# Optimization experiments

Measured on AMD Instinct MI355X. Metric: run time of the kernel, lower is better.

Reference implementation:

```python
import jax, jax.numpy as jnp
import numpy as np

ROPE_BASE = 10000.0

def rope_2d(x, h, w):
    # x: (b, h, w, c); 2D RoPE, first half of pair-channels rotated by row angle, second by col angle
    b, _, _, c = x.shape
    k_max = c // 4  # c // (2 * num_spatial_dims)
    theta = 1.0 / (ROPE_BASE ** (jnp.arange(k_max, dtype=jnp.float32) / k_max))  # (k_max,)
    ang_h = jnp.arange(h, dtype=jnp.float32)[:, None] * theta  # (h, k_max)
    ang_w = jnp.arange(w, dtype=jnp.float32)[:, None] * theta  # (w, k_max)
    # angles: (h, w, 2*k_max) = cat([i*theta, j*theta], -1)
    angles = jnp.concatenate([
        jnp.broadcast_to(ang_h[:, None, :], (h, w, k_max)),
        jnp.broadcast_to(ang_w[None, :, :], (h, w, k_max)),
    ], axis=-1)
    cos = jnp.cos(angles)  # (h, w, c//2)
    sin = jnp.sin(angles)
    xr = x[..., 0::2]  # consecutive-pair real parts (b,h,w,c//2)
    xi = x[..., 1::2]
    out_r = xr * cos - xi * sin
    out_i = xr * sin + xi * cos
    return jnp.stack([out_r, out_i], axis=-1).reshape(b, h, w, c)

def linear_attention_fwd(x, h, w, qk_w, qk_b, lepe_w, lepe_b, num_heads=4):
    b, n, c = x.shape
    head_dim = c // num_heads
    qk = x @ qk_w.T + qk_b  # (b, n, 2c)
    q, k = qk[..., :c], qk[..., c:]
    v = x
    q = jax.nn.elu(q) + 1.0
    k = jax.nn.elu(k) + 1.0
    q_rope = rope_2d(q.reshape(b, h, w, c), h, w).reshape(b, n, num_heads, head_dim).transpose(0, 2, 1, 3)
    k_rope = rope_2d(k.reshape(b, h, w, c), h, w).reshape(b, n, num_heads, head_dim).transpose(0, 2, 1, 3)
    qh = q.reshape(b, n, num_heads, head_dim).transpose(0, 2, 1, 3)  # (b,H,n,d)
    kh = k.reshape(b, n, num_heads, head_dim).transpose(0, 2, 1, 3)
    vh = v.reshape(b, n, num_heads, head_dim).transpose(0, 2, 1, 3)
    k_mean = kh.mean(axis=2)  # (b,H,d)
    z = 1.0 / (jnp.einsum('bhnd,bhd->bhn', qh, k_mean) + 1e-6)  # (b,H,n)
    inv_n = 1.0 / n
    kv = jnp.einsum('bhnd,bhne->bhde', k_rope, vh) * inv_n  # (b,H,d,d)
    out = jnp.einsum('bhnd,bhde->bhne', q_rope, kv) * z[..., None]  # (b,H,n,d)
    out = out.transpose(0, 2, 1, 3).reshape(b, n, c)
    # LePE: depthwise 3x3 conv on v in NCHW
    v_img = v.reshape(b, h, w, c).transpose(0, 3, 1, 2)  # (b,c,h,w)
    lepe = jax.lax.conv_general_dilated(
        v_img, lepe_w, window_strides=(1, 1), padding='SAME',
        feature_group_count=c, dimension_numbers=('NCHW', 'OIHW', 'NCHW'))
    lepe = lepe + lepe_b[None, :, None, None]
    out = out + lepe.transpose(0, 2, 3, 1).reshape(b, n, c)
    return out.transpose(0, 2, 1).reshape(b, c, h, w)

def setup_inputs() -> dict:
    key = jax.random.key(0)
    ks = jax.random.split(key, 5)
    b, h, w, c = 16, 128, 128, 64
    n = h * w
    x = jax.random.normal(ks[0], (b, n, c), dtype=jnp.float32)
    qk_w = jax.random.normal(ks[1], (2 * c, c), dtype=jnp.float32) * (1.0 / np.sqrt(c))
    qk_b = jax.random.normal(ks[2], (2 * c,), dtype=jnp.float32) * 0.02
    lepe_w = jax.random.normal(ks[3], (c, 1, 3, 3), dtype=jnp.float32) * (1.0 / 3.0)
    lepe_b = jax.random.normal(ks[4], (c,), dtype=jnp.float32) * 0.02
    return {"x": x, "h": h, "w": w, "qk_w": qk_w, "qk_b": qk_b, "lepe_w": lepe_w, "lepe_b": lepe_b}

def reference(x, h, w, qk_w, qk_b, lepe_w, lepe_b):
    return linear_attention_fwd(x, h, w, qk_w, qk_b, lepe_w, lepe_b, num_heads=4)
```

## Files before the change

### kernel.cpp

```cpp
#include <hip/hip_runtime.h>

#define B_   16
#define C_   64
#define HH   128
#define WW   128
#define NN   (HH*WW)
#define NH   4
#define PADB 72
#define PADO 66

typedef short short8 __attribute__((ext_vector_type(8)));
typedef float f32x4  __attribute__((ext_vector_type(4)));

#define NEG_L2_10K_OVER16 (-0.8304820237218406f)

__device__ __forceinline__ float act_elu1(float v) {
    return v > 0.f ? v + 1.f : __expf(v);
}
__device__ __forceinline__ short f2bf(float f) {
    union { float f; unsigned u; } v; v.f = f;
    unsigned r = (v.u + 0x7FFFu + ((v.u >> 16) & 1u)) >> 16;
    return (short)r;
}
__device__ __forceinline__ float bf2f(short s) {
    union { unsigned u; float f; } v; v.u = ((unsigned)(unsigned short)s) << 16;
    return v.f;
}
__device__ __forceinline__ unsigned cvt2bf(float lo, float hi) {
    unsigned r;
    asm("v_cvt_pk_bf16_f32 %0, %1, %2" : "=v"(r) : "v"(lo), "v"(hi));
    return r;
}

__global__ __launch_bounds__(256) void la_init(
    const float* __restrict__ qk_w, const float* __restrict__ lepe_w,
    float2* __restrict__ g_tab, float* __restrict__ g_wT,
    short* __restrict__ g_wbf)
{
    int i = blockIdx.x * 256 + threadIdx.x;
    g_wbf[i] = f2bf(qk_w[i]);
    if (i < 2048) {
        int coord = i >> 4, t = i & 15;
        float theta = exp2f(NEG_L2_10K_OVER16 * (float)t);
        float s, c;
        __sincosf((float)coord * theta, &s, &c);
        g_tab[i] = make_float2(c, s);
    }
    if (i < 576) {
        int tap = i >> 6, ch = i & 63;
        g_wT[i] = lepe_w[ch * 9 + tap];
    }
}

__global__ __launch_bounds__(256) void la_phase1(
    const float* __restrict__ x, const float* __restrict__ qk_b,
    const short* __restrict__ g_wbf, const float2* __restrict__ g_tab,
    float* __restrict__ g_part, short* __restrict__ g_q)
{
    __shared__ __align__(16) char pool[3*64*PADB*2 + 256*4];
    short* sXT = (short*)pool;
    short* sKT = sXT + 64*PADB;
    short* sQ  = sKT + 64*PADB;
    float* kmp = (float*)(sQ + 64*PADB);

    const int tid  = threadIdx.x;
    const int w    = tid >> 6;
    const int ln   = tid & 15;
    const int quad = (tid >> 4) & 3;
    const int b    = blockIdx.y;
    const int nblk = blockIdx.x;
    const float* xb = x + (size_t)b * (size_t)(NN * C_);

    float biasK[4], biasQ[4];
    #pragma unroll
    for (int nt = 0; nt < 4; ++nt) {
        biasK[nt] = qk_b[64 + 16*nt + ln];
        biasQ[nt] = qk_b[16*nt + ln];
    }

    f32x4 acc2 = {0.f, 0.f, 0.f, 0.f};
    float kmacc[4] = {0.f, 0.f, 0.f, 0.f};

    for (int ck = 0; ck < 4; ++ck) {
        const int n0 = nblk*256 + ck*64;
        if (ck) __syncthreads();
        #pragma unroll
        for (int it = 0; it < 4; ++it) {
            int idx = tid + 256*it;
            int row = idx & 63, k4 = (idx >> 6) << 2;
            float4 xv = *(const float4*)(xb + (size_t)(n0 + row)*C_ + k4);
            unsigned p01 = cvt2bf(xv.x, xv.y), p23 = cvt2bf(xv.z, xv.w);
            sXT[(k4+0)*PADB + row] = (short)p01;
            sXT[(k4+1)*PADB + row] = (short)(p01 >> 16);
            sXT[(k4+2)*PADB + row] = (short)p23;
            sXT[(k4+3)*PADB + row] = (short)(p23 >> 16);
        }
        short8 aF[2];
        #pragma unroll
        for (int ks = 0; ks < 2; ++ks) {
            const float* ap = xb + (size_t)(n0 + 16*w + ln)*C_ + 32*ks + 8*quad;
            float4 a0 = *(const float4*)ap;
            float4 a1 = *(const float4*)(ap + 4);
            union { unsigned u[4]; short8 s; } af;
            af.u[0] = cvt2bf(a0.x, a0.y);
            af.u[1] = cvt2bf(a0.z, a0.w);
            af.u[2] = cvt2bf(a1.x, a1.y);
            af.u[3] = cvt2bf(a1.z, a1.w);
            aF[ks] = af.s;
        }
        f32x4 ak[4], aq[4];
        #pragma unroll
        for (int nt = 0; nt < 4; ++nt) { ak[nt] = (f32x4){0.f,0.f,0.f,0.f}; aq[nt] = (f32x4){0.f,0.f,0.f,0.f}; }
        #pragma unroll
        for (int ks = 0; ks < 2; ++ks) {
            #pragma unroll
            for (int nt = 0; nt < 4; ++nt) {
                short8 bk = *(const short8*)(g_wbf + (64 + 16*nt + ln)*C_ + 32*ks + 8*quad);
                short8 bq = *(const short8*)(g_wbf + (16*nt + ln)*C_ + 32*ks + 8*quad);
                ak[nt] = __builtin_amdgcn_mfma_f32_16x16x32_bf16(aF[ks], bk, ak[nt], 0, 0, 0);
                aq[nt] = __builtin_amdgcn_mfma_f32_16x16x32_bf16(aF[ks], bq, aq[nt], 0, 0, 0);
            }
        }
        const int ycoord = n0 >> 7;
        const int x0 = n0 & 127;
        #pragma unroll
        for (int nt = 0; nt < 4; ++nt) {
            const int j = 16*nt + ln;
            const int t = j >> 1;
            const float sgn = (j & 1) ? 1.f : -1.f;
            float2 cs_y;
            if (nt < 2) cs_y = g_tab[ycoord*16 + t];
            #pragma unroll
            for (int r = 0; r < 4; ++r) {
                int p_loc = 16*w + 4*quad + r;
                float kval = act_elu1(ak[nt][r] + biasK[nt]);
                kmacc[nt] += kval;
                float P = __shfl_xor(kval, 1);
                float2 cs = (nt < 2) ? cs_y : g_tab[(x0 + p_loc)*16 + (t - 16)];
                float kr = kval*cs.x + sgn*P*cs.y;
                sKT[j*PADB + p_loc] = f2bf(kr);
                float qval = act_elu1(aq[nt][r] + biasQ[nt]);
                sQ[p_loc*PADB + j] = f2bf(qval);
            }
        }
        __syncthreads();
        #pragma unroll
        for (int ks = 0; ks < 2; ++ks) {
            short8 a  = *(const short8*)(sKT + (16*w + ln)*PADB + 32*ks + 8*quad);
            short8 bf = *(const short8*)(sXT + (16*w + ln)*PADB + 32*ks + 8*quad);
            acc2 = __builtin_amdgcn_mfma_f32_16x16x32_bf16(a, bf, acc2, 0, 0, 0);
        }
        #pragma unroll
        for (int cp = 0; cp < 2; ++cp) {
            int idx = tid + 256*cp;
            int row = idx >> 3, c8 = idx & 7;
            short8 qv = *(const short8*)(sQ + row*PADB + 8*c8);
            *(short8*)(g_q + ((size_t)b*NN + n0 + row)*C_ + 8*c8) = qv;
        }
    }

    float* pb = g_part + (size_t)(b*64 + nblk) * 1088;
    #pragma unroll
    for (int r = 0; r < 4; ++r)
        pb[w*256 + (4*quad + r)*16 + ln] = acc2[r];

    #pragma unroll
    for (int nt = 0; nt < 4; ++nt) {
        float v = kmacc[nt];
        v += __shfl_xor(v, 16);
        v += __shfl_xor(v, 32);
        if ((tid & 63) < 16) kmp[w*64 + 16*nt + ln] = v;
    }
    __syncthreads();
    if (tid < 64)
        pb[1024 + tid] = kmp[tid] + kmp[64 + tid] + kmp[128 + tid] + kmp[192 + tid];
}

__global__ __launch_bounds__(256) void la_reduce(
    const float* __restrict__ g_part, float* __restrict__ g_kv,
    float* __restrict__ g_km)
{
    int o = blockIdx.x * 256 + threadIdx.x;
    int b = o / 1088;
    int i = o - b * 1088;
    const float* p = g_part + (size_t)(b*64) * 1088 + i;
    float s = 0.f;
    #pragma unroll 8
    for (int nb = 0; nb < 64; ++nb) s += p[(size_t)nb * 1088];
    if (i < 1024) g_kv[b*1024 + i] = s;
    else          g_km[b*64 + (i - 1024)] = s;
}

__global__ __launch_bounds__(256) void la_phase2(
    const float* __restrict__ x, const short* __restrict__ g_q,
    const float* __restrict__ g_kv, const float* __restrict__ g_km,
    const float2* __restrict__ g_tab, const float* __restrict__ g_wT,
    const float* __restrict__ lepe_b, float* __restrict__ out)
{
    __shared__ __align__(16) char pool[64*40*2 + 64*PADO*4];
    short* sKVB = (short*)pool;
    float* sOut = (float*)(pool + 64*40*2);

    const int tid  = threadIdx.x;
    const int w    = tid >> 6;
    const int ln   = tid & 15;
    const int quad = (tid >> 4) & 3;
    const int b    = blockIdx.y;
    const int n0   = blockIdx.x * 64;
    const float* xb = x + (size_t)b * (size_t)(NN * C_);
    const float inv_n = 1.f / (float)NN;

    for (int idx = tid; idx < 1024; idx += 256) {
        int h = idx >> 8, d = (idx >> 4) & 15, e = idx & 15;
        float v = g_kv[b*1024 + idx] * inv_n;
        int rowb = h*16 + e;
        int kpos  = (h & 1) ? 16 + d : d;
        int kzero = (h & 1) ? d : 16 + d;
        sKVB[rowb*40 + kpos]  = f2bf(v);
        sKVB[rowb*40 + kzero] = 0;
    }

    const int pos    = n0 + 16*w + ln;
    const int ycoord = n0 >> 7;
    const int xcoord = (n0 & 127) + 16*w + ln;
    const short* qp = g_q + ((size_t)b*NN + pos)*C_;
    short8 q0 = *(const short8*)(qp + 8*quad);
    short8 q1 = *(const short8*)(qp + 32 + 8*quad);
    float qa[8], qb[8];
    #pragma unroll
    for (int i = 0; i < 8; ++i) { qa[i] = bf2f(q0[i]); qb[i] = bf2f(q1[i]); }

    const float* kmb = g_km + b*64;
    f32x4 km0 = *(const f32x4*)(kmb + 8*quad);
    f32x4 km1 = *(const f32x4*)(kmb + 8*quad + 4);
    f32x4 km2 = *(const f32x4*)(kmb + 32 + 8*quad);
    f32x4 km3 = *(const f32x4*)(kmb + 32 + 8*quad + 4);
    float d0 = 0.f, d1 = 0.f;
    #pragma unroll
    for (int i = 0; i < 4; ++i) {
        d0 += qa[i]*km0[i] + qa[4+i]*km1[i];
        d1 += qb[i]*km2[i] + qb[4+i]*km3[i];
    }
    d0 += __shfl_xor(d0, 16);
    d1 += __shfl_xor(d1, 16);
    const float z0 = 1.f / (d0*inv_n + 1e-6f);
    const float z1 = 1.f / (d1*inv_n + 1e-6f);

    const float* tyP = (const float*)g_tab + (ycoord*16 + 4*quad)*2;
    const float* txP = (const float*)g_tab + (xcoord*16 + 4*quad)*2;
    f32x4 ty0 = *(const f32x4*)tyP, ty1 = *(const f32x4*)(tyP + 4);
    f32x4 tx0 = *(const f32x4*)txP, tx1 = *(const f32x4*)(txP + 4);
    float cy[4] = {ty0[0], ty0[2], ty1[0], ty1[2]};
    float sy[4] = {ty0[1], ty0[3], ty1[1], ty1[3]};
    float cx[4] = {tx0[0], tx0[2], tx1[0], tx1[2]};
    float sx[4] = {tx0[1], tx0[3], tx1[1], tx1[3]};
    union { unsigned u[4]; short8 s; } A0, A1;
    #pragma unroll
    for (int p = 0; p < 4; ++p) {
        float e0 = qa[2*p], o0 = qa[2*p+1];
        A0.u[p] = cvt2bf((e0*cy[p] - o0*sy[p])*z0, (e0*sy[p] + o0*cy[p])*z0);
        float e1 = qb[2*p], o1 = qb[2*p+1];
        A1.u[p] = cvt2bf((e1*cx[p] - o1*sx[p])*z1, (e1*sx[p] + o1*cx[p])*z1);
    }

    __syncthreads();

    f32x4 accq[4];
    #pragma unroll
    for (int h = 0; h < 4; ++h) accq[h] = (f32x4){0.f,0.f,0.f,0.f};
    #pragma unroll
    for (int hh = 0; hh < 2; ++hh) {
        short8 bf0 = *(const short8*)(sKVB + (hh*16 + ln)*40 + 8*quad);
        accq[hh]   = __builtin_amdgcn_mfma_f32_16x16x32_bf16(A0.s, bf0, accq[hh], 0, 0, 0);
        short8 bf1 = *(const short8*)(sKVB + ((2+hh)*16 + ln)*40 + 8*quad);
        accq[2+hh] = __builtin_amdgcn_mfma_f32_16x16x32_bf16(A1.s, bf1, accq[2+hh], 0, 0, 0);
    }
    #pragma unroll
    for (int h = 0; h < 4; ++h)
        #pragma unroll
        for (int r = 0; r < 4; ++r)
            sOut[(16*h + ln)*PADO + 16*w + 4*quad + r] = accq[h][r];

    const int cg = tid & 15;
    const int pg = tid >> 4;
    const int p0 = 4*pg;
    const int yy = n0 >> 7, xbase = n0 & 127, gx0 = xbase + p0;
    f32x4 accl[4];
    #pragma unroll
    for (int j = 0; j < 4; ++j) accl[j] = (f32x4){0.f,0.f,0.f,0.f};
    #pragma unroll
    for (int dy = -1; dy <= 1; ++dy) {
        int y2 = yy + dy;
        if ((unsigned)y2 >= HH) continue;
        f32x4 wt0 = *(const f32x4*)(g_wT + ((dy+1)*3 + 0)*C_ + 4*cg);
        f32x4 wt1 = *(const f32x4*)(g_wT + ((dy+1)*3 + 1)*C_ + 4*cg);
        f32x4 wt2 = *(const f32x4*)(g_wT + ((dy+1)*3 + 2)*C_ + 4*cg);
        const float* rp = xb + (size_t)(y2*WW)*C_ + 4*cg;
        f32x4 cb[6];
        #pragma unroll
        for (int jj = 0; jj < 6; ++jj) {
            int col = gx0 - 1 + jj;
            cb[jj] = ((unsigned)col < WW) ? *(const f32x4*)(rp + (size_t)col*C_)
                                          : (f32x4){0.f,0.f,0.f,0.f};
        }
        #pragma unroll
        for (int j = 0; j < 4; ++j)
            accl[j] += cb[j]*wt0 + cb[j+1]*wt1 + cb[j+2]*wt2;
    }
    __syncthreads();
    #pragma unroll
    for (int j = 0; j < 4; ++j)
        #pragma unroll
        for (int i = 0; i < 4; ++i)
            sOut[(4*cg + i)*PADO + p0 + j] += accl[j][i];
    __syncthreads();

    const int ch = tid >> 2, sub = tid & 3, pp0 = 16*sub;
    const float lb = lepe_b[ch];
    float* outp = out + (size_t)b*(size_t)(C_*NN) + (size_t)ch*NN + n0 + pp0;
    #pragma unroll
    for (int g = 0; g < 4; ++g) {
        float2 a0 = *(const float2*)(sOut + ch*PADO + pp0 + 4*g);
        float2 a1 = *(const float2*)(sOut + ch*PADO + pp0 + 4*g + 2);
        float4 o4 = { a0.x + lb, a0.y + lb, a1.x + lb, a1.y + lb };
        *(float4*)(outp + 4*g) = o4;
    }
}

extern "C" void kernel_launch(void* const* d_in, const int* in_sizes, int n_in,
                              void* d_out, int out_size, void* d_ws, size_t ws_size,
                              hipStream_t stream) {
    const float* x      = (const float*)d_in[0];
    const float* qk_w   = (const float*)d_in[3];
    const float* qk_b   = (const float*)d_in[4];
    const float* lepe_w = (const float*)d_in[5];
    const float* lepe_b = (const float*)d_in[6];
    float* out = (float*)d_out;

    float*  g_part = (float*)d_ws;
    float*  g_kv   = g_part + 1024*1088;
    float*  g_km   = g_kv + 16*1024;
    float2* g_tab  = (float2*)(g_km + 16*64);
    float*  g_wT   = (float*)(g_tab + 2048);
    short*  g_wbf  = (short*)(g_wT + 576);
    short*  g_q    = (short*)(g_wbf + 8192);

    hipLaunchKernelGGL(la_init,   dim3(32),      dim3(256), 0, stream,
                       qk_w, lepe_w, g_tab, g_wT, g_wbf);
    hipLaunchKernelGGL(la_phase1, dim3(64, B_),  dim3(256), 0, stream,
                       x, qk_b, g_wbf, g_tab, g_part, g_q);
    hipLaunchKernelGGL(la_reduce, dim3(68),      dim3(256), 0, stream,
                       g_part, g_kv, g_km);
    hipLaunchKernelGGL(la_phase2, dim3(256, B_), dim3(256), 0, stream,
                       x, g_q, g_kv, g_km, g_tab, g_wT, lepe_b, out);
}
```

Before: 216.6 us.

## Recompute Q in phase2, atomically reduce KV, and drop init and reduce kernels

Phase 1 now computes only K, accumulates KV and k-mean directly with global atomics, and uses twice as many blocks. Phase 2 recomputes Q from x with its own MFMA projection, which removes the bf16 Q round trip through global memory. RoPE angles come from hardware sin/cos instead of a precomputed table, and the init and reduce kernels are replaced by a memset. The cost is redundant weight conversion in every block, extra atomic contention, and sin/cos accuracy that depends on range reduction.

```diff
diff --git a/kernel.cpp b/kernel.cpp
--- a/kernel.cpp
+++ b/kernel.cpp
@@ -5,7 +5,6 @@
 #define HH   128
 #define WW   128
 #define NN   (HH*WW)
-#define NH   4
 #define PADB 72
 #define PADO 66
 
@@ -13,6 +12,7 @@
 typedef float f32x4  __attribute__((ext_vector_type(4)));
 
 #define NEG_L2_10K_OVER16 (-0.8304820237218406f)
+#define INV2PI 0.15915494309189535f
 
 __device__ __forceinline__ float act_elu1(float v) {
     return v > 0.f ? v + 1.f : __expf(v);
@@ -22,46 +22,26 @@
     unsigned r = (v.u + 0x7FFFu + ((v.u >> 16) & 1u)) >> 16;
     return (short)r;
 }
-__device__ __forceinline__ float bf2f(short s) {
-    union { unsigned u; float f; } v; v.u = ((unsigned)(unsigned short)s) << 16;
-    return v.f;
-}
 __device__ __forceinline__ unsigned cvt2bf(float lo, float hi) {
     unsigned r;
     asm("v_cvt_pk_bf16_f32 %0, %1, %2" : "=v"(r) : "v"(lo), "v"(hi));
     return r;
 }
-
-__global__ __launch_bounds__(256) void la_init(
-    const float* __restrict__ qk_w, const float* __restrict__ lepe_w,
-    float2* __restrict__ g_tab, float* __restrict__ g_wT,
-    short* __restrict__ g_wbf)
+__device__ __forceinline__ void hw_sincos(float rev, float* s, float* c) {
+    float f = rev - floorf(rev);
+    *s = __builtin_amdgcn_sinf(f);
+    *c = __builtin_amdgcn_cosf(f);
+}
+
+__global__ __launch_bounds__(256) void la_phase1(
+    const float* __restrict__ x, const float* __restrict__ qk_w,
+    const float* __restrict__ qk_b, float* __restrict__ g_kv,
+    float* __restrict__ g_km)
 {
-    int i = blockIdx.x * 256 + threadIdx.x;
-    g_wbf[i] = f2bf(qk_w[i]);
-    if (i < 2048) {
-        int coord = i >> 4, t = i & 15;
-        float theta = exp2f(NEG_L2_10K_OVER16 * (float)t);
-        float s, c;
-        __sincosf((float)coord * theta, &s, &c);
-        g_tab[i] = make_float2(c, s);
-    }
-    if (i < 576) {
-        int tap = i >> 6, ch = i & 63;
-        g_wT[i] = lepe_w[ch * 9 + tap];
-    }
-}
-
-__global__ __launch_bounds__(256) void la_phase1(
-    const float* __restrict__ x, const float* __restrict__ qk_b,
-    const short* __restrict__ g_wbf, const float2* __restrict__ g_tab,
-    float* __restrict__ g_part, short* __restrict__ g_q)
-{
-    __shared__ __align__(16) char pool[3*64*PADB*2 + 256*4];
+    __shared__ __align__(16) char pool[2*64*PADB*2 + 256*4];
     short* sXT = (short*)pool;
     short* sKT = sXT + 64*PADB;
-    short* sQ  = sKT + 64*PADB;
-    float* kmp = (float*)(sQ + 64*PADB);
+    float* kmp = (float*)(sKT + 64*PADB);
 
     const int tid  = threadIdx.x;
     const int w    = tid >> 6;
@@ -71,18 +51,36 @@
     const int nblk = blockIdx.x;
     const float* xb = x + (size_t)b * (size_t)(NN * C_);
 
-    float biasK[4], biasQ[4];
-    #pragma unroll
-    for (int nt = 0; nt < 4; ++nt) {
-        biasK[nt] = qk_b[64 + 16*nt + ln];
-        biasQ[nt] = qk_b[16*nt + ln];
-    }
+    short8 bk[2][4];
+    #pragma unroll
+    for (int ks = 0; ks < 2; ++ks)
+        #pragma unroll
+        for (int nt = 0; nt < 4; ++nt) {
+            const float* wp = qk_w + (64 + 16*nt + ln)*C_ + 32*ks + 8*quad;
+            float4 w0 = *(const float4*)wp, w1 = *(const float4*)(wp + 4);
+            union { unsigned u[4]; short8 s; } uf;
+            uf.u[0] = cvt2bf(w0.x, w0.y); uf.u[1] = cvt2bf(w0.z, w0.w);
+            uf.u[2] = cvt2bf(w1.x, w1.y); uf.u[3] = cvt2bf(w1.z, w1.w);
+            bk[ks][nt] = uf.s;
+        }
+    float biasK[4];
+    #pragma unroll
+    for (int nt = 0; nt < 4; ++nt) biasK[nt] = qk_b[64 + 16*nt + ln];
+
+    float th[2];
+    #pragma unroll
+    for (int i = 0; i < 2; ++i)
+        th[i] = exp2f(NEG_L2_10K_OVER16 * (float)(8*i + (ln >> 1))) * INV2PI;
+    float sy[2], cy[2];
+    #pragma unroll
+    for (int i = 0; i < 2; ++i) hw_sincos((float)nblk * th[i], &sy[i], &cy[i]);
 
     f32x4 acc2 = {0.f, 0.f, 0.f, 0.f};
     float kmacc[4] = {0.f, 0.f, 0.f, 0.f};
-
-    for (int ck = 0; ck < 4; ++ck) {
-        const int n0 = nblk*256 + ck*64;
+    const int p_base = 16*w + 4*quad;
+
+    for (int ck = 0; ck < 2; ++ck) {
+        const int n0 = nblk*128 + ck*64;
         if (ck) __syncthreads();
         #pragma unroll
         for (int it = 0; it < 4; ++it) {
@@ -108,39 +106,30 @@
             af.u[3] = cvt2bf(a1.z, a1.w);
             aF[ks] = af.s;
         }
-        f32x4 ak[4], aq[4];
-        #pragma unroll
-        for (int nt = 0; nt < 4; ++nt) { ak[nt] = (f32x4){0.f,0.f,0.f,0.f}; aq[nt] = (f32x4){0.f,0.f,0.f,0.f}; }
-        #pragma unroll
-        for (int ks = 0; ks < 2; ++ks) {
+        f32x4 ak[4];
+        #pragma unroll
+        for (int nt = 0; nt < 4; ++nt) ak[nt] = (f32x4){0.f,0.f,0.f,0.f};
+        #pragma unroll
+        for (int ks = 0; ks < 2; ++ks)
             #pragma unroll
-            for (int nt = 0; nt < 4; ++nt) {
-                short8 bk = *(const short8*)(g_wbf + (64 + 16*nt + ln)*C_ + 32*ks + 8*quad);
-                short8 bq = *(const short8*)(g_wbf + (16*nt + ln)*C_ + 32*ks + 8*quad);
-                ak[nt] = __builtin_amdgcn_mfma_f32_16x16x32_bf16(aF[ks], bk, ak[nt], 0, 0, 0);
-                aq[nt] = __builtin_amdgcn_mfma_f32_16x16x32_bf16(aF[ks], bq, aq[nt], 0, 0, 0);
-            }
-        }
-        const int ycoord = n0 >> 7;
-        const int x0 = n0 & 127;
+            for (int nt = 0; nt < 4; ++nt)
+                ak[nt] = __builtin_amdgcn_mfma_f32_16x16x32_bf16(aF[ks], bk[ks][nt], ak[nt], 0, 0, 0);
+
+        const int x0 = ck*64;
         #pragma unroll
         for (int nt = 0; nt < 4; ++nt) {
             const int j = 16*nt + ln;
-            const int t = j >> 1;
             const float sgn = (j & 1) ? 1.f : -1.f;
-            float2 cs_y;
-            if (nt < 2) cs_y = g_tab[ycoord*16 + t];
             #pragma unroll
             for (int r = 0; r < 4; ++r) {
-                int p_loc = 16*w + 4*quad + r;
+                int p_loc = p_base + r;
                 float kval = act_elu1(ak[nt][r] + biasK[nt]);
                 kmacc[nt] += kval;
                 float P = __shfl_xor(kval, 1);
-                float2 cs = (nt < 2) ? cs_y : g_tab[(x0 + p_loc)*16 + (t - 16)];
-                float kr = kval*cs.x + sgn*P*cs.y;
-                sKT[j*PADB + p_loc] = f2bf(kr);
-                float qval = act_elu1(aq[nt][r] + biasQ[nt]);
-                sQ[p_loc*PADB + j] = f2bf(qval);
+                float s, c;
+                if (nt < 2) { s = sy[nt]; c = cy[nt]; }
+                else hw_sincos((float)(x0 + p_loc) * th[nt & 1], &s, &c);
+                sKT[j*PADB + p_loc] = f2bf(kval*c + sgn*P*s);
             }
         }
         __syncthreads();
@@ -150,19 +139,12 @@
             short8 bf = *(const short8*)(sXT + (16*w + ln)*PADB + 32*ks + 8*quad);
             acc2 = __builtin_amdgcn_mfma_f32_16x16x32_bf16(a, bf, acc2, 0, 0, 0);
         }
-        #pragma unroll
-        for (int cp = 0; cp < 2; ++cp) {
-            int idx = tid + 256*cp;
-            int row = idx >> 3, c8 = idx & 7;
-            short8 qv = *(const short8*)(sQ + row*PADB + 8*c8);
-            *(short8*)(g_q + ((size_t)b*NN + n0 + row)*C_ + 8*c8) = qv;
-        }
-    }
-
-    float* pb = g_part + (size_t)(b*64 + nblk) * 1088;
+    }
+
+    float* kvb = g_kv + b*1024;
     #pragma unroll
     for (int r = 0; r < 4; ++r)
-        pb[w*256 + (4*quad + r)*16 + ln] = acc2[r];
+        atomicAdd(kvb + w*256 + (4*quad + r)*16 + ln, acc2[r]);
 
     #pragma unroll
     for (int nt = 0; nt < 4; ++nt) {
@@ -173,33 +155,21 @@
     }
     __syncthreads();
     if (tid < 64)
-        pb[1024 + tid] = kmp[tid] + kmp[64 + tid] + kmp[128 + tid] + kmp[192 + tid];
-}
-
-__global__ __launch_bounds__(256) void la_reduce(
-    const float* __restrict__ g_part, float* __restrict__ g_kv,
-    float* __restrict__ g_km)
+        atomicAdd(g_km + b*64 + tid,
+                  kmp[tid] + kmp[64 + tid] + kmp[128 + tid] + kmp[192 + tid]);
+}
+
+__global__ __launch_bounds__(256) void la_phase2(
+    const float* __restrict__ x, const float* __restrict__ qk_w,
+    const float* __restrict__ qk_b, const float* __restrict__ lepe_w,
+    const float* __restrict__ lepe_b, const float* __restrict__ g_kv,
+    const float* __restrict__ g_km, float* __restrict__ out)
 {
-    int o = blockIdx.x * 256 + threadIdx.x;
-    int b = o / 1088;
-    int i = o - b * 1088;
-    const float* p = g_part + (size_t)(b*64) * 1088 + i;
-    float s = 0.f;
-    #pragma unroll 8
-    for (int nb = 0; nb < 64; ++nb) s += p[(size_t)nb * 1088];
-    if (i < 1024) g_kv[b*1024 + i] = s;
-    else          g_km[b*64 + (i - 1024)] = s;
-}
-
-__global__ __launch_bounds__(256) void la_phase2(
-    const float* __restrict__ x, const short* __restrict__ g_q,
-    const float* __restrict__ g_kv, const float* __restrict__ g_km,
-    const float2* __restrict__ g_tab, const float* __restrict__ g_wT,
-    const float* __restrict__ lepe_b, float* __restrict__ out)
-{
-    __shared__ __align__(16) char pool[64*40*2 + 64*PADO*4];
+    __shared__ __align__(16) char pool[5120 + 9216 + 16896 + 2304];
     short* sKVB = (short*)pool;
-    float* sOut = (float*)(pool + 64*40*2);
+    short* sQ   = (short*)(pool + 5120);
+    float* sOut = (float*)(pool + 5120 + 9216);
+    float* sWT  = (float*)(pool + 5120 + 9216 + 16896);
 
     const int tid  = threadIdx.x;
     const int w    = tid >> 6;
@@ -219,61 +189,114 @@
         sKVB[rowb*40 + kpos]  = f2bf(v);
         sKVB[rowb*40 + kzero] = 0;
     }
-
-    const int pos    = n0 + 16*w + ln;
+    if (tid < 144) {
+        float4 lw = *(const float4*)(lepe_w + tid*4);
+        float lwv[4] = {lw.x, lw.y, lw.z, lw.w};
+        #pragma unroll
+        for (int i = 0; i < 4; ++i) {
+            int e = tid*4 + i, ch = e / 9, tap = e - ch*9;
+            sWT[tap*64 + ch] = lwv[i];
+        }
+    }
+
+    short8 wq[2][4];
+    #pragma unroll
+    for (int ks = 0; ks < 2; ++ks)
+        #pragma unroll
+        for (int nt = 0; nt < 4; ++nt) {
+            const float* wp = qk_w + (16*nt + ln)*C_ + 32*ks + 8*quad;
+            float4 w0 = *(const float4*)wp, w1 = *(const float4*)(wp + 4);
+            union { unsigned u[4]; short8 s; } uf;
+            uf.u[0] = cvt2bf(w0.x, w0.y); uf.u[1] = cvt2bf(w0.z, w0.w);
+            uf.u[2] = cvt2bf(w1.x, w1.y); uf.u[3] = cvt2bf(w1.z, w1.w);
+            wq[ks][nt] = uf.s;
+        }
+    float biasq[4], kmv[4];
+    #pragma unroll
+    for (int nt = 0; nt < 4; ++nt) {
+        biasq[nt] = qk_b[16*nt + ln];
+        kmv[nt]   = g_km[b*64 + 16*nt + ln];
+    }
+    short8 aF[2];
+    #pragma unroll
+    for (int ks = 0; ks < 2; ++ks) {
+        const float* ap = xb + (size_t)(n0 + 16*w + ln)*C_ + 32*ks + 8*quad;
+        float4 a0 = *(const float4*)ap;
+        float4 a1 = *(const float4*)(ap + 4);
+        union { unsigned u[4]; short8 s; } af;
+        af.u[0] = cvt2bf(a0.x, a0.y);
+        af.u[1] = cvt2bf(a0.z, a0.w);
+        af.u[2] = cvt2bf(a1.x, a1.y);
+        af.u[3] = cvt2bf(a1.z, a1.w);
+        aF[ks] = af.s;
+    }
+    f32x4 aq[4];
+    #pragma unroll
+    for (int nt = 0; nt < 4; ++nt) aq[nt] = (f32x4){0.f,0.f,0.f,0.f};
+    #pragma unroll
+    for (int ks = 0; ks < 2; ++ks)
+        #pragma unroll
+        for (int nt = 0; nt < 4; ++nt)
+            aq[nt] = __builtin_amdgcn_mfma_f32_16x16x32_bf16(aF[ks], wq[ks][nt], aq[nt], 0, 0, 0);
+
+    float qv[4][4], dot[4] = {0.f, 0.f, 0.f, 0.f};
+    #pragma unroll
+    for (int nt = 0; nt < 4; ++nt)
+        #pragma unroll
+        for (int r = 0; r < 4; ++r) {
+            qv[nt][r] = act_elu1(aq[nt][r] + biasq[nt]);
+            dot[r] += qv[nt][r] * kmv[nt];
+        }
+    float zr[4];
+    #pragma unroll
+    for (int r = 0; r < 4; ++r) {
+        float d = dot[r];
+        d += __shfl_xor(d, 1);
+        d += __shfl_xor(d, 2);
+        d += __shfl_xor(d, 4);
+        d += __shfl_xor(d, 8);
+        zr[r] = 1.f / (d * inv_n + 1e-6f);
+    }
+
+    float th[2];
+    #pragma unroll
+    for (int i = 0; i < 2; ++i)
+        th[i] = exp2f(NEG_L2_10K_OVER16 * (float)(8*i + (ln >> 1))) * INV2PI;
     const int ycoord = n0 >> 7;
-    const int xcoord = (n0 & 127) + 16*w + ln;
-    const short* qp = g_q + ((size_t)b*NN + pos)*C_;
-    short8 q0 = *(const short8*)(qp + 8*quad);
-    short8 q1 = *(const short8*)(qp + 32 + 8*quad);
-    float qa[8], qb[8];
-    #pragma unroll
-    for (int i = 0; i < 8; ++i) { qa[i] = bf2f(q0[i]); qb[i] = bf2f(q1[i]); }
-
-    const float* kmb = g_km + b*64;
-    f32x4 km0 = *(const f32x4*)(kmb + 8*quad);
-    f32x4 km1 = *(const f32x4*)(kmb + 8*quad + 4);
-    f32x4 km2 = *(const f32x4*)(kmb + 32 + 8*quad);
-    f32x4 km3 = *(const f32x4*)(kmb + 32 + 8*quad + 4);
-    float d0 = 0.f, d1 = 0.f;
-    #pragma unroll
-    for (int i = 0; i < 4; ++i) {
-        d0 += qa[i]*km0[i] + qa[4+i]*km1[i];
-        d1 += qb[i]*km2[i] + qb[4+i]*km3[i];
-    }
-    d0 += __shfl_xor(d0, 16);
-    d1 += __shfl_xor(d1, 16);
-    const float z0 = 1.f / (d0*inv_n + 1e-6f);
-    const float z1 = 1.f / (d1*inv_n + 1e-6f);
-
-    const float* tyP = (const float*)g_tab + (ycoord*16 + 4*quad)*2;
-    const float* txP = (const float*)g_tab + (xcoord*16 + 4*quad)*2;
-    f32x4 ty0 = *(const f32x4*)tyP, ty1 = *(const f32x4*)(tyP + 4);
-    f32x4 tx0 = *(const f32x4*)txP, tx1 = *(const f32x4*)(txP + 4);
-    float cy[4] = {ty0[0], ty0[2], ty1[0], ty1[2]};
-    float sy[4] = {ty0[1], ty0[3], ty1[1], ty1[3]};
-    float cx[4] = {tx0[0], tx0[2], tx1[0], tx1[2]};
-    float sx[4] = {tx0[1], tx0[3], tx1[1], tx1[3]};
-    union { unsigned u[4]; short8 s; } A0, A1;
-    #pragma unroll
-    for (int p = 0; p < 4; ++p) {
-        float e0 = qa[2*p], o0 = qa[2*p+1];
-        A0.u[p] = cvt2bf((e0*cy[p] - o0*sy[p])*z0, (e0*sy[p] + o0*cy[p])*z0);
-        float e1 = qb[2*p], o1 = qb[2*p+1];
-        A1.u[p] = cvt2bf((e1*cx[p] - o1*sx[p])*z1, (e1*sx[p] + o1*cx[p])*z1);
-    }
-
+    const int x0 = n0 & 127;
+    float sy[2], cy[2];
+    #pragma unroll
+    for (int i = 0; i < 2; ++i) hw_sincos((float)ycoord * th[i], &sy[i], &cy[i]);
+    const int p_base = 16*w + 4*quad;
+    #pragma unroll
+    for (int nt = 0; nt < 4; ++nt) {
+        const int j = 16*nt + ln;
+        const float sgn = (j & 1) ? 1.f : -1.f;
+        #pragma unroll
+        for (int r = 0; r < 4; ++r) {
+            int p_loc = p_base + r;
+            float s, c;
+            if (nt < 2) { s = sy[nt]; c = cy[nt]; }
+            else hw_sincos((float)(x0 + p_loc) * th[nt & 1], &s, &c);
+            float P = __shfl_xor(qv[nt][r], 1);
+            float qr = (qv[nt][r]*c + sgn*P*s) * zr[r];
+            sQ[p_loc*PADB + j] = f2bf(qr);
+        }
+    }
     __syncthreads();
 
     f32x4 accq[4];
     #pragma unroll
     for (int h = 0; h < 4; ++h) accq[h] = (f32x4){0.f,0.f,0.f,0.f};
     #pragma unroll
-    for (int hh = 0; hh < 2; ++hh) {
-        short8 bf0 = *(const short8*)(sKVB + (hh*16 + ln)*40 + 8*quad);
-        accq[hh]   = __builtin_amdgcn_mfma_f32_16x16x32_bf16(A0.s, bf0, accq[hh], 0, 0, 0);
-        short8 bf1 = *(const short8*)(sKVB + ((2+hh)*16 + ln)*40 + 8*quad);
-        accq[2+hh] = __builtin_amdgcn_mfma_f32_16x16x32_bf16(A1.s, bf1, accq[2+hh], 0, 0, 0);
+    for (int P2 = 0; P2 < 2; ++P2) {
+        short8 a = *(const short8*)(sQ + (16*w + ln)*PADB + 32*P2 + 8*quad);
+        #pragma unroll
+        for (int hh = 0; hh < 2; ++hh) {
+            int h = 2*P2 + hh;
+            short8 bf = *(const short8*)(sKVB + (h*16 + ln)*40 + 8*quad);
+            accq[h] = __builtin_amdgcn_mfma_f32_16x16x32_bf16(a, bf, accq[h], 0, 0, 0);
+        }
     }
     #pragma unroll
     for (int h = 0; h < 4; ++h)
@@ -292,9 +315,9 @@
     for (int dy = -1; dy <= 1; ++dy) {
         int y2 = yy + dy;
         if ((unsigned)y2 >= HH) continue;
-        f32x4 wt0 = *(const f32x4*)(g_wT + ((dy+1)*3 + 0)*C_ + 4*cg);
-        f32x4 wt1 = *(const f32x4*)(g_wT + ((dy+1)*3 + 1)*C_ + 4*cg);
-        f32x4 wt2 = *(const f32x4*)(g_wT + ((dy+1)*3 + 2)*C_ + 4*cg);
+        f32x4 wt0 = *(const f32x4*)(sWT + ((dy+1)*3 + 0)*C_ + 4*cg);
+        f32x4 wt1 = *(const f32x4*)(sWT + ((dy+1)*3 + 1)*C_ + 4*cg);
+        f32x4 wt2 = *(const f32x4*)(sWT + ((dy+1)*3 + 2)*C_ + 4*cg);
         const float* rp = xb + (size_t)(y2*WW)*C_ + 4*cg;
         f32x4 cb[6];
         #pragma unroll
@@ -337,20 +360,12 @@
     const float* lepe_b = (const float*)d_in[6];
     float* out = (float*)d_out;
 
-    float*  g_part = (float*)d_ws;
-    float*  g_kv   = g_part + 1024*1088;
-    float*  g_km   = g_kv + 16*1024;
-    float2* g_tab  = (float2*)(g_km + 16*64);
-    float*  g_wT   = (float*)(g_tab + 2048);
-    short*  g_wbf  = (short*)(g_wT + 576);
-    short*  g_q    = (short*)(g_wbf + 8192);
-
-    hipLaunchKernelGGL(la_init,   dim3(32),      dim3(256), 0, stream,
-                       qk_w, lepe_w, g_tab, g_wT, g_wbf);
-    hipLaunchKernelGGL(la_phase1, dim3(64, B_),  dim3(256), 0, stream,
-                       x, qk_b, g_wbf, g_tab, g_part, g_q);
-    hipLaunchKernelGGL(la_reduce, dim3(68),      dim3(256), 0, stream,
-                       g_part, g_kv, g_km);
+    float* g_kv = (float*)d_ws;
+    float* g_km = g_kv + 16*1024;
+    hipMemsetAsync(d_ws, 0, (size_t)(16*1024 + 16*64) * sizeof(float), stream);
+
+    hipLaunchKernelGGL(la_phase1, dim3(128, B_), dim3(256), 0, stream,
+                       x, qk_w, qk_b, g_kv, g_km);
     hipLaunchKernelGGL(la_phase2, dim3(256, B_), dim3(256), 0, stream,
-                       x, g_q, g_kv, g_km, g_tab, g_wT, lepe_b, out);
-}
+                       x, qk_w, qk_b, lepe_w, lepe_b, g_kv, g_km, out);
+}
```

Result: faster. 210.6 us (-2.7%).
